# Kernel tuning notes

Hardware: AMD Instinct MI355X
Metric: run time of the kernel (lower is better)

Reference implementation:

```python
import jax, jax.numpy as jnp
import numpy as np

N_ATOMS = 128
BATCH = 512


def _build_buffers(n):
    # Segments: all non-adjacent bond pairs (i,i+1,j,j+1), j >= i+2, j+1 <= n-1.
    segs = np.array([(i, i + 1, j, j + 1)
                     for i in range(n - 3)
                     for j in range(i + 2, n - 1)], dtype=np.int32)  # (S,4)

    def pidx(a, b):  # linear index of pair (a,b), a<b, in row-major triu(offset=1) order
        return a * n - a * (a + 1) // 2 + (b - a - 1)

    # Each writhe value scatters into its 4 incident residue pairs.
    # Pairs (0,1) [triu idx 0] and (n-2,n-1) [last triu idx] are never incident,
    # so ranks among interior pairs are (triu idx - 1); they are re-inserted by pad.
    inc = []
    for (i, _, j, _) in segs:
        for (a, b) in ((i, j), (i, j + 1), (i + 1, j), (i + 1, j + 1)):
            inc.append(pidx(a, b) - 1)
    indices = np.array(inc, dtype=np.int32)  # (4*S,)

    # Sort permutation placing [upper-triu values, lower-triu values] into
    # row-major order of all off-diagonal (r,c) entries, keyed by r*n + c.
    iu = np.stack(np.triu_indices(n, 1))  # (2, P) row-major
    vals = np.concatenate([iu[0] * n + iu[1], iu[1] * n + iu[0]])
    sort = np.argsort(vals).astype(np.int32)  # (n^2 - n,)
    return segs, indices, sort


def setup_inputs() -> dict:
    key = jax.random.key(0)
    xyz = jax.random.normal(key, (BATCH, N_ATOMS, 3), dtype=jnp.float32)
    segs, indices, sort = _build_buffers(N_ATOMS)
    return {
        "xyz": xyz,
        "segments": jnp.asarray(segs),
        "indices": jnp.asarray(indices),
        "sort": jnp.asarray(sort),
    }


def _divnorm(x):
    return x / jnp.linalg.norm(x, axis=-1, keepdims=True)


def _writhe(xyz, segments):
    # xyz: (B,N,3); segments: (S,4) -> writhe per segment pair, (B,S)
    B, S = xyz.shape[0], segments.shape[0]
    p = xyz[:, segments]  # (B,S,4,3) gathered endpoints [s1a,s1b,s2a,s2b]
    # d[k] = normalize(p_{2+j} - p_i), k = 2*i + j  (the 4 inter-segment directions)
    d = _divnorm((p[:, :, None, 2:, :] - p[:, :, :2, None, :]).reshape(B, S, 4, 3))
    axial = jnp.cross(p[:, :, 3] - p[:, :, 2], p[:, :, 1] - p[:, :, 0])  # (B,S,3)
    signs = jnp.sign(jnp.sum(axial * d[:, :, 0], -1))  # (B,S)
    # 4 face normals of the spherical quadrilateral, then Gauss-Bonnet angle sum
    nrm = _divnorm(jnp.cross(d[:, :, jnp.array([0, 1, 3, 2])],
                             d[:, :, jnp.array([1, 3, 2, 0])]))  # (B,S,4,3)
    cosang = jnp.clip(jnp.sum(nrm * nrm[:, :, jnp.array([1, 2, 3, 0])], -1), -1.0, 1.0)
    omega = jnp.arcsin(cosang).sum(-1)  # (B,S)
    return omega * signs / (2.0 * jnp.pi)


def _laplacian(wr, indices, sort, n):
    # wr: (B,S); scatter-add each writhe into its 4 incident residue pairs,
    # pad back the two untouched pairs, symmetrize, and sort into row-major
    # off-diagonal order -> (B, n^2 - n)
    M = (n * n - n) // 2 - 2
    triu = jnp.zeros((wr.shape[0], M), wr.dtype).at[:, indices].add(
        jnp.repeat(wr, 4, axis=1))
    padded = jnp.pad(triu, ((0, 0), (1, 1)))
    return jnp.concatenate([padded, padded], axis=1)[:, sort]


def reference(xyz, segments, indices, sort):
    xyz = xyz.reshape(-1, N_ATOMS, 3)
    wr = _writhe(xyz, segments)
    return _laplacian(wr, indices, sort, N_ATOMS)
```

## Files before the change

kernel.cpp:

```cpp
#include <hip/hip_runtime.h>
#include <math.h>

#define NATOMS    128
#define NSEG      7875
#define NSEG_PAD  8192
#define NPAIR     8128
#define OUT_PER_B 16256
#define BLOCK     512

typedef float v2f __attribute__((ext_vector_type(2)));
__device__ __forceinline__ v2f mk2(float a, float b) { v2f r; r.x = a; r.y = b; return r; }

struct P3 { v2f x, y, z; };
__device__ __forceinline__ P3 psub(P3 a, P3 b) { return {a.x - b.x, a.y - b.y, a.z - b.z}; }
__device__ __forceinline__ P3 pcross(P3 a, P3 b) {
    return {a.y * b.z - a.z * b.y, a.z * b.x - a.x * b.z, a.x * b.y - a.y * b.x};
}
__device__ __forceinline__ v2f pdot(P3 a, P3 b) { return a.x * b.x + a.y * b.y + a.z * b.z; }
__device__ __forceinline__ v2f prsq(v2f q) {
    v2f r; r.x = __builtin_amdgcn_rsqf(q.x); r.y = __builtin_amdgcn_rsqf(q.y); return r;
}
__device__ __forceinline__ v2f pclip1(v2f x) {
    return __builtin_elementwise_min(__builtin_elementwise_max(x, mk2(-1.f, -1.f)),
                                     mk2(1.f, 1.f));
}

__device__ __forceinline__ v2f fast_asin2(v2f x) {
    v2f a = __builtin_elementwise_abs(x);
    v2f p = mk2(-0.0187293f, -0.0187293f);
    p = p * a + mk2( 0.0742610f,  0.0742610f);
    p = p * a + mk2(-0.2121144f, -0.2121144f);
    p = p * a + mk2( 1.5707288f,  1.5707288f);
    v2f om = mk2(1.0f, 1.0f) - a;
    v2f sq; sq.x = __builtin_amdgcn_sqrtf(om.x); sq.y = __builtin_amdgcn_sqrtf(om.y);
    v2f r = mk2(1.57079632679f, 1.57079632679f) - sq * p;
    return __builtin_elementwise_copysign(r, x);
}

__device__ __forceinline__ int seg_row_base(int i) { return 125 * i - (__umul24(i, i - 1) >> 1); }

__device__ __forceinline__ P3 pack3(const float4 &a, const float4 &b) {
    return { mk2(a.x, b.x), mk2(a.y, b.y), mk2(a.z, b.z) };
}

__device__ __forceinline__ v2f seg_writhe_pair(unsigned pa, unsigned pb,
                                               const float4* sp4) {
    int jA = (int)(pa & 127u), iA = (int)(pa >> 7);
    int jB = (int)(pb & 127u), iB = (int)(pb >> 7);

    float4 A0 = sp4[iA], A1 = sp4[iA + 1], A2 = sp4[jA], A3 = sp4[jA + 1];
    float4 B0 = sp4[iB], B1 = sp4[iB + 1], B2 = sp4[jB], B3 = sp4[jB + 1];

    P3 p0 = pack3(A0, B0);
    P3 p1 = pack3(A1, B1);
    P3 p2 = pack3(A2, B2);
    P3 p3 = pack3(A3, B3);

    P3 u0 = psub(p2, p0);
    P3 u1 = psub(p3, p0);
    P3 u2 = psub(p2, p1);
    P3 u3 = psub(p3, p1);

    P3 n0 = pcross(u0, u1);
    P3 n1 = pcross(u1, u3);
    P3 n2 = pcross(u3, u2);
    P3 n3 = pcross(u2, u0);

    v2f q0 = pdot(n0, n0);
    v2f q1 = pdot(n1, n1);
    v2f q2 = pdot(n2, n2);
    v2f q3 = pdot(n3, n3);

    v2f c0 = pclip1(pdot(n0, n1) * prsq(q0 * q1));
    v2f c1 = pclip1(pdot(n1, n2) * prsq(q1 * q2));
    v2f c2 = pclip1(pdot(n2, n3) * prsq(q2 * q3));
    v2f c3 = pclip1(pdot(n3, n0) * prsq(q3 * q0));

    v2f sd = pdot(n2, u0);
    v2f omega = fast_asin2(c0) + fast_asin2(c1) + fast_asin2(c2) + fast_asin2(c3);

    v2f sgn;
    sgn.x = (sd.x > 0.f) ? -1.f : ((sd.x < 0.f) ? 1.f : 0.f);
    sgn.y = (sd.y > 0.f) ? -1.f : ((sd.y < 0.f) ? 1.f : 0.f);

    return omega * sgn * mk2(0.15915494309189535f, 0.15915494309189535f);
}

__global__ __launch_bounds__(BLOCK, 4) void writhe_fused(
    const float* __restrict__ xyz,
    float*       __restrict__ out)
{
    __shared__ float4 sp4[NATOMS];
    __shared__ float  swr[NSEG_PAD];
    __shared__ unsigned short sidx[NSEG_PAD];

    const int b = blockIdx.x;
    const int t = threadIdx.x;

    if (t < 3 * NATOMS) {
        float v = xyz[(size_t)b * (3 * NATOMS) + t];
        int a = t / 3, c = t - 3 * a;
        ((float*)&sp4[a])[c] = v;
    }

    {
        int s = t * 16;
        if (s < NSEG) {
            int i = (int)((251.0f - __builtin_amdgcn_sqrtf(63001.0f - 8.0f * (float)s)) * 0.5f);
            i = max(i, 0);
            i += (seg_row_base(i + 1) <= s);
            i += (seg_row_base(i + 1) <= s);
            i -= (seg_row_base(i) > s);
            i -= (seg_row_base(i) > s);
            int j = s - seg_row_base(i) + i + 2;
            #pragma unroll
            for (int k = 0; k < 16; ++k) {
                if (s < NSEG) sidx[s] = (unsigned short)((i << 7) | j);
                ++s; ++j;
                if (j > 126) { ++i; j = i + 2; }
            }
        }
        if (t < NSEG_PAD - NSEG) sidx[NSEG + t] = (unsigned short)((124 << 7) | 126);
    }
    __syncthreads();

    #pragma unroll
    for (int g = 0; g < 4; ++g) {
        const int sA = g * 2048 + t;
        v2f w1 = seg_writhe_pair(sidx[sA],        sidx[sA + 512],  sp4);
        v2f w2 = seg_writhe_pair(sidx[sA + 1024], sidx[sA + 1536], sp4);
        swr[sA]        = w1.x;
        swr[sA + 512]  = w1.y;
        swr[sA + 1024] = w2.x;
        swr[sA + 1536] = w2.y;
    }
    __syncthreads();

    float* ob = out + (size_t)b * OUT_PER_B;
    for (int k = t; k < OUT_PER_B; k += BLOCK) {
        const int r = (int)(((unsigned)k * 132105u) >> 24);
        int c = k - r * 127;
        c += (c >= r);
        const int a  = min(r, c);
        const int bb = max(r, c);

        const int am1 = a - 1;
        const int s00 = 125 * am1 - ((am1 * (am1 - 1)) >> 1) + bb - a - 2;
        const int s10 = s00 + 125 - a;

        const bool v00 = (a >= 1) && (a <= 125) && (bb >= a + 2);
        const bool v01 = (a >= 1) && (a <= 125) && (bb <= 126);
        const bool v10 = (a <= 124) && (bb >= a + 3);
        const bool v11 = (a <= 124) && (bb <= 126) && (bb >= a + 2);

        const int c00 = min(max(s00,     0), NSEG - 1);
        const int c01 = min(max(s00 + 1, 0), NSEG - 1);
        const int c10 = min(max(s10,     0), NSEG - 1);
        const int c11 = min(max(s10 + 1, 0), NSEG - 1);

        float sum = (v00 ? swr[c00] : 0.0f) + (v01 ? swr[c01] : 0.0f)
                  + (v10 ? swr[c10] : 0.0f) + (v11 ? swr[c11] : 0.0f);

        __builtin_nontemporal_store(sum, ob + k);
    }
}

extern "C" void kernel_launch(void* const* d_in, const int* in_sizes, int n_in,
                              void* d_out, int out_size, void* d_ws, size_t ws_size,
                              hipStream_t stream) {
    const float* xyz = (const float*)d_in[0];
    float*       out = (float*)d_out;

    int B = in_sizes[0] / (NATOMS * 3);
    writhe_fused<<<B, BLOCK, 0, stream>>>(xyz, out);
}
```

Baseline: 92.28 us.

## Split fused writhe kernel into segment and gather kernels via workspace

After: 130.5 us. +41.4%, slower.

```diff
diff --git a/kernel.cpp b/kernel.cpp
--- a/kernel.cpp
+++ b/kernel.cpp
@@ -4,19 +4,138 @@
 #define NATOMS    128
 #define NSEG      7875
 #define NSEG_PAD  8192
-#define NPAIR     8128
 #define OUT_PER_B 16256
 #define BLOCK     512
 
 typedef float v2f __attribute__((ext_vector_type(2)));
 __device__ __forceinline__ v2f mk2(float a, float b) { v2f r; r.x = a; r.y = b; return r; }
 
-struct P3 { v2f x, y, z; };
-__device__ __forceinline__ P3 psub(P3 a, P3 b) { return {a.x - b.x, a.y - b.y, a.z - b.z}; }
-__device__ __forceinline__ P3 pcross(P3 a, P3 b) {
+struct F3 { float x, y, z; };
+__device__ __forceinline__ F3 f3(float x, float y, float z) { F3 r; r.x = x; r.y = y; r.z = z; return r; }
+__device__ __forceinline__ F3 fsub(F3 a, F3 b) { return f3(a.x - b.x, a.y - b.y, a.z - b.z); }
+__device__ __forceinline__ F3 fcross(F3 a, F3 b) {
+    return f3(a.y * b.z - a.z * b.y, a.z * b.x - a.x * b.z, a.x * b.y - a.y * b.x);
+}
+__device__ __forceinline__ float fdot(F3 a, F3 b) { return a.x * b.x + a.y * b.y + a.z * b.z; }
+__device__ __forceinline__ float fclip1(float x) { return fminf(fmaxf(x, -1.f), 1.f); }
+
+__device__ __forceinline__ float fast_asin(float x) {
+    float a = fabsf(x);
+    float p = -0.0187293f;
+    p = p * a + 0.0742610f;
+    p = p * a + -0.2121144f;
+    p = p * a + 1.5707288f;
+    float r = 1.57079632679f - __builtin_amdgcn_sqrtf(1.0f - a) * p;
+    return copysignf(r, x);
+}
+
+__device__ __forceinline__ int seg_row_base(int i) { return 125 * i - (__umul24(i, i - 1) >> 1); }
+
+__device__ __forceinline__ void seed_ij(int s, int &i, int &j) {
+    i = (int)((251.0f - __builtin_amdgcn_sqrtf(63001.0f - 8.0f * (float)s)) * 0.5f);
+    i = max(i, 0);
+    i += (seg_row_base(i + 1) <= s);
+    i += (seg_row_base(i + 1) <= s);
+    i -= (seg_row_base(i) > s);
+    i -= (seg_row_base(i) > s);
+    j = s - seg_row_base(i) + i + 2;
+}
+
+__global__ __launch_bounds__(256) void writhe_seg(
+    const float* __restrict__ xyz,
+    float*       __restrict__ ws)
+{
+    __shared__ float4 sp4[NATOMS];
+    const int bid = blockIdx.x;
+    const int b   = bid >> 5;
+    const int sb  = bid & 31;
+    const int t   = threadIdx.x;
+
+    if (t < NATOMS) {
+        const float* src = xyz + (size_t)b * (3 * NATOMS) + 3 * t;
+        sp4[t] = make_float4(src[0], src[1], src[2], 0.f);
+    }
+    __syncthreads();
+
+    const int s = (sb << 8) | t;
+    if (s >= NSEG) return;
+
+    int i, j; seed_ij(s, i, j);
+
+    float4 P0 = sp4[i], P1 = sp4[i + 1], P2 = sp4[j], P3 = sp4[j + 1];
+    F3 p0 = f3(P0.x, P0.y, P0.z), p1 = f3(P1.x, P1.y, P1.z);
+    F3 p2 = f3(P2.x, P2.y, P2.z), p3 = f3(P3.x, P3.y, P3.z);
+
+    F3 u0 = fsub(p2, p0);
+    F3 u1 = fsub(p3, p0);
+    F3 u2 = fsub(p2, p1);
+    F3 u3 = fsub(p3, p1);
+
+    F3 n0 = fcross(u0, u1);
+    F3 n1 = fcross(u1, u3);
+    F3 n2 = fcross(u3, u2);
+    F3 n3 = fcross(u2, u0);
+
+    float q0 = fdot(n0, n0);
+    float q1 = fdot(n1, n1);
+    float q2 = fdot(n2, n2);
+    float q3 = fdot(n3, n3);
+
+    float c0 = fclip1(fdot(n0, n1) * __builtin_amdgcn_rsqf(q0 * q1));
+    float c1 = fclip1(fdot(n1, n2) * __builtin_amdgcn_rsqf(q1 * q2));
+    float c2 = fclip1(fdot(n2, n3) * __builtin_amdgcn_rsqf(q2 * q3));
+    float c3 = fclip1(fdot(n3, n0) * __builtin_amdgcn_rsqf(q3 * q0));
+
+    float sd = fdot(n2, u0);
+    float omega = fast_asin(c0) + fast_asin(c1) + fast_asin(c2) + fast_asin(c3);
+    float sgn = (sd > 0.f) ? -1.f : ((sd < 0.f) ? 1.f : 0.f);
+
+    ws[(size_t)b * NSEG_PAD + s] = omega * sgn * 0.15915494309189535f;
+}
+
+__global__ __launch_bounds__(256) void writhe_gather(
+    const float* __restrict__ ws,
+    float*       __restrict__ out)
+{
+    const int bid = blockIdx.x;
+    const int b   = bid >> 6;
+    const int k   = ((bid & 63) << 8) | threadIdx.x;
+    if (k >= OUT_PER_B) return;
+
+    const float* w = ws + (size_t)b * NSEG_PAD;
+
+    const int r = (int)(((unsigned)k * 132105u) >> 24);
+    int c = k - r * 127;
+    c += (c >= r);
+    const int a  = min(r, c);
+    const int bb = max(r, c);
+
+    const int am1 = a - 1;
+    const int s00 = 125 * am1 - ((am1 * (am1 - 1)) >> 1) + bb - a - 2;
+    const int s10 = s00 + 125 - a;
+
+    const bool v00 = (a >= 1) && (a <= 125) && (bb >= a + 2);
+    const bool v01 = (a >= 1) && (a <= 125) && (bb <= 126);
+    const bool v10 = (a <= 124) && (bb >= a + 3);
+    const bool v11 = (a <= 124) && (bb <= 126) && (bb >= a + 2);
+
+    const int c00 = min(max(s00,     0), NSEG - 1);
+    const int c01 = min(max(s00 + 1, 0), NSEG - 1);
+    const int c10 = min(max(s10,     0), NSEG - 1);
+    const int c11 = min(max(s10 + 1, 0), NSEG - 1);
+
+    float sum = (v00 ? w[c00] : 0.0f) + (v01 ? w[c01] : 0.0f)
+              + (v10 ? w[c10] : 0.0f) + (v11 ? w[c11] : 0.0f);
+
+    __builtin_nontemporal_store(sum, out + (size_t)b * OUT_PER_B + k);
+}
+
+struct P3p { v2f x, y, z; };
+__device__ __forceinline__ P3p psub(P3p a, P3p b) { return {a.x - b.x, a.y - b.y, a.z - b.z}; }
+__device__ __forceinline__ P3p pcross(P3p a, P3p b) {
     return {a.y * b.z - a.z * b.y, a.z * b.x - a.x * b.z, a.x * b.y - a.y * b.x};
 }
-__device__ __forceinline__ v2f pdot(P3 a, P3 b) { return a.x * b.x + a.y * b.y + a.z * b.z; }
+__device__ __forceinline__ v2f pdot(P3p a, P3p b) { return a.x * b.x + a.y * b.y + a.z * b.z; }
 __device__ __forceinline__ v2f prsq(v2f q) {
     v2f r; r.x = __builtin_amdgcn_rsqf(q.x); r.y = __builtin_amdgcn_rsqf(q.y); return r;
 }
@@ -24,7 +143,6 @@
     return __builtin_elementwise_min(__builtin_elementwise_max(x, mk2(-1.f, -1.f)),
                                      mk2(1.f, 1.f));
 }
-
 __device__ __forceinline__ v2f fast_asin2(v2f x) {
     v2f a = __builtin_elementwise_abs(x);
     v2f p = mk2(-0.0187293f, -0.0187293f);
@@ -36,83 +154,47 @@
     v2f r = mk2(1.57079632679f, 1.57079632679f) - sq * p;
     return __builtin_elementwise_copysign(r, x);
 }
-
-__device__ __forceinline__ int seg_row_base(int i) { return 125 * i - (__umul24(i, i - 1) >> 1); }
-
-__device__ __forceinline__ P3 pack3(const float4 &a, const float4 &b) {
+__device__ __forceinline__ P3p pack3(const float4 &a, const float4 &b) {
     return { mk2(a.x, b.x), mk2(a.y, b.y), mk2(a.z, b.z) };
 }
-
-__device__ __forceinline__ v2f seg_writhe_pair(unsigned pa, unsigned pb,
-                                               const float4* sp4) {
+__device__ __forceinline__ v2f seg_writhe_pair(unsigned pa, unsigned pb, const float4* sp4) {
     int jA = (int)(pa & 127u), iA = (int)(pa >> 7);
     int jB = (int)(pb & 127u), iB = (int)(pb >> 7);
-
     float4 A0 = sp4[iA], A1 = sp4[iA + 1], A2 = sp4[jA], A3 = sp4[jA + 1];
     float4 B0 = sp4[iB], B1 = sp4[iB + 1], B2 = sp4[jB], B3 = sp4[jB + 1];
-
-    P3 p0 = pack3(A0, B0);
-    P3 p1 = pack3(A1, B1);
-    P3 p2 = pack3(A2, B2);
-    P3 p3 = pack3(A3, B3);
-
-    P3 u0 = psub(p2, p0);
-    P3 u1 = psub(p3, p0);
-    P3 u2 = psub(p2, p1);
-    P3 u3 = psub(p3, p1);
-
-    P3 n0 = pcross(u0, u1);
-    P3 n1 = pcross(u1, u3);
-    P3 n2 = pcross(u3, u2);
-    P3 n3 = pcross(u2, u0);
-
-    v2f q0 = pdot(n0, n0);
-    v2f q1 = pdot(n1, n1);
-    v2f q2 = pdot(n2, n2);
-    v2f q3 = pdot(n3, n3);
-
+    P3p p0 = pack3(A0, B0), p1 = pack3(A1, B1), p2 = pack3(A2, B2), p3 = pack3(A3, B3);
+    P3p u0 = psub(p2, p0), u1 = psub(p3, p0), u2 = psub(p2, p1), u3 = psub(p3, p1);
+    P3p n0 = pcross(u0, u1), n1 = pcross(u1, u3), n2 = pcross(u3, u2), n3 = pcross(u2, u0);
+    v2f q0 = pdot(n0, n0), q1 = pdot(n1, n1), q2 = pdot(n2, n2), q3 = pdot(n3, n3);
     v2f c0 = pclip1(pdot(n0, n1) * prsq(q0 * q1));
     v2f c1 = pclip1(pdot(n1, n2) * prsq(q1 * q2));
     v2f c2 = pclip1(pdot(n2, n3) * prsq(q2 * q3));
     v2f c3 = pclip1(pdot(n3, n0) * prsq(q3 * q0));
-
     v2f sd = pdot(n2, u0);
     v2f omega = fast_asin2(c0) + fast_asin2(c1) + fast_asin2(c2) + fast_asin2(c3);
-
     v2f sgn;
     sgn.x = (sd.x > 0.f) ? -1.f : ((sd.x < 0.f) ? 1.f : 0.f);
     sgn.y = (sd.y > 0.f) ? -1.f : ((sd.y < 0.f) ? 1.f : 0.f);
-
     return omega * sgn * mk2(0.15915494309189535f, 0.15915494309189535f);
 }
 
 __global__ __launch_bounds__(BLOCK, 4) void writhe_fused(
-    const float* __restrict__ xyz,
-    float*       __restrict__ out)
+    const float* __restrict__ xyz, float* __restrict__ out)
 {
     __shared__ float4 sp4[NATOMS];
     __shared__ float  swr[NSEG_PAD];
     __shared__ unsigned short sidx[NSEG_PAD];
-
     const int b = blockIdx.x;
     const int t = threadIdx.x;
-
     if (t < 3 * NATOMS) {
         float v = xyz[(size_t)b * (3 * NATOMS) + t];
         int a = t / 3, c = t - 3 * a;
         ((float*)&sp4[a])[c] = v;
     }
-
     {
         int s = t * 16;
         if (s < NSEG) {
-            int i = (int)((251.0f - __builtin_amdgcn_sqrtf(63001.0f - 8.0f * (float)s)) * 0.5f);
-            i = max(i, 0);
-            i += (seg_row_base(i + 1) <= s);
-            i += (seg_row_base(i + 1) <= s);
-            i -= (seg_row_base(i) > s);
-            i -= (seg_row_base(i) > s);
-            int j = s - seg_row_base(i) + i + 2;
+            int i, j; seed_ij(s, i, j);
             #pragma unroll
             for (int k = 0; k < 16; ++k) {
                 if (s < NSEG) sidx[s] = (unsigned short)((i << 7) | j);
@@ -123,7 +205,6 @@
         if (t < NSEG_PAD - NSEG) sidx[NSEG + t] = (unsigned short)((124 << 7) | 126);
     }
     __syncthreads();
-
     #pragma unroll
     for (int g = 0; g < 4; ++g) {
         const int sA = g * 2048 + t;
@@ -135,7 +216,6 @@
         swr[sA + 1536] = w2.y;
     }
     __syncthreads();
-
     float* ob = out + (size_t)b * OUT_PER_B;
     for (int k = t; k < OUT_PER_B; k += BLOCK) {
         const int r = (int)(((unsigned)k * 132105u) >> 24);
@@ -143,24 +223,19 @@
         c += (c >= r);
         const int a  = min(r, c);
         const int bb = max(r, c);
-
         const int am1 = a - 1;
         const int s00 = 125 * am1 - ((am1 * (am1 - 1)) >> 1) + bb - a - 2;
         const int s10 = s00 + 125 - a;
-
         const bool v00 = (a >= 1) && (a <= 125) && (bb >= a + 2);
         const bool v01 = (a >= 1) && (a <= 125) && (bb <= 126);
         const bool v10 = (a <= 124) && (bb >= a + 3);
         const bool v11 = (a <= 124) && (bb <= 126) && (bb >= a + 2);
-
         const int c00 = min(max(s00,     0), NSEG - 1);
         const int c01 = min(max(s00 + 1, 0), NSEG - 1);
         const int c10 = min(max(s10,     0), NSEG - 1);
         const int c11 = min(max(s10 + 1, 0), NSEG - 1);
-
         float sum = (v00 ? swr[c00] : 0.0f) + (v01 ? swr[c01] : 0.0f)
                   + (v10 ? swr[c10] : 0.0f) + (v11 ? swr[c11] : 0.0f);
-
         __builtin_nontemporal_store(sum, ob + k);
     }
 }
@@ -172,5 +247,13 @@
     float*       out = (float*)d_out;
 
     int B = in_sizes[0] / (NATOMS * 3);
-    writhe_fused<<<B, BLOCK, 0, stream>>>(xyz, out);
-}
+
+    const size_t need = (size_t)B * NSEG_PAD * sizeof(float);
+    if (d_ws != nullptr && ws_size >= need) {
+        float* ws = (float*)d_ws;
+        writhe_seg<<<B * 32, 256, 0, stream>>>(xyz, ws);
+        writhe_gather<<<B * 64, 256, 0, stream>>>(ws, out);
+    } else {
+        writhe_fused<<<B, BLOCK, 0, stream>>>(xyz, out);
+    }
+}
```
